# Kernel tuning notes

Measured on AMD Instinct MI355X. Metric: run time of the kernel, lower is better.

## Reference

```python
import jax, jax.numpy as jnp
import numpy as np

N = 100000   # nodes
E = 3200000  # edges
F = 128      # input features
H1 = 128     # first_gcn_dimensions
H2 = 64      # second_gcn_dimensions
D1 = 64      # first_dense_neurons
D2 = 8       # second_dense_neurons
L = 10       # number_of_labels


def setup_inputs() -> dict:
    key = jax.random.key(0)
    ks = jax.random.split(key, 8)
    edges = jax.random.randint(ks[0], (2, E), 0, N)
    features = jax.random.normal(ks[1], (N, F), dtype=jnp.float32)
    s = lambda k, shape: jax.random.normal(k, shape, dtype=jnp.float32) * 0.05
    return dict(
        edges=edges, features=features,
        W1=s(ks[2], (F, H1)), b1=jnp.zeros((H1,), jnp.float32),
        W2=s(ks[3], (H1, H2)), b2=jnp.zeros((H2,), jnp.float32),
        Wf1=s(ks[4], (H2, D1)), bf1=jnp.zeros((D1,), jnp.float32),
        Wf2=s(ks[5], (D1, D2)), bf2=jnp.zeros((D2,), jnp.float32),
        Wl=s(ks[6], (H2 * D2, L)), bl=jnp.zeros((L,), jnp.float32),
    )


def gcn_conv(x, W, b, src, dst, n):
    # PyG GCNConv: x' = D^{-1/2} (A + I) D^{-1/2} (x W) + b  (self-loops already in src/dst)
    h = x @ W                                            # [N, out]
    deg = jax.ops.segment_sum(jnp.ones(dst.shape[0], x.dtype), dst, num_segments=n)
    dinv = jnp.where(deg > 0, jax.lax.rsqrt(deg), 0.0)   # deg^{-1/2}, 0 for isolated
    norm = dinv[src] * dinv[dst]                         # [E+N]
    agg = jax.ops.segment_sum(h[src] * norm[:, None], dst, num_segments=n)
    return agg + b


def reference(edges, features, W1, b1, W2, b2, Wf1, bf1, Wf2, bf2, Wl, bl):
    n = features.shape[0]
    loop = jnp.arange(n)
    src = jnp.concatenate([edges[0], loop])
    dst = jnp.concatenate([edges[1], loop])

    h1 = jax.nn.relu(gcn_conv(features, W1, b1, src, dst, n))  # [N, H1]
    h2 = gcn_conv(h1, W2, b2, src, dst, n)                     # [N, H2]

    a1 = jnp.tanh(h2 @ Wf1 + bf1)                              # [N, D1]
    att = jax.nn.softmax(a1 @ Wf2 + bf2, axis=0)               # softmax over nodes, [N, D2]

    graph_embedding = (att.T @ h2).reshape(1, -1)              # [1, D2*H2]
    P = att.T @ att - jnp.eye(att.shape[1], dtype=att.dtype)   # [D2, D2]
    penalty = jnp.sum(jnp.sqrt(jnp.sum(P * P, axis=1)))

    predictions = jax.nn.log_softmax(graph_embedding @ Wl + bl, axis=1)  # [1, L]
    return graph_embedding, penalty, predictions
```

## Files before the change

kernel.cpp:

```cpp
#include <hip/hip_runtime.h>
#include <hip/hip_bf16.h>
#include <math.h>

#define NNODES 100000
#define NEDGES 3200000
#define NBUK ((NNODES + 127) >> 7)
#define NCHUNK 256
#define EPC (NEDGES / NCHUNK)
#define NPAD 100352
#define SLICEB ((size_t)NPAD * 32)

typedef float floatx2 __attribute__((ext_vector_type(2)));
typedef float f32x4 __attribute__((ext_vector_type(4)));
typedef short bf16x8 __attribute__((ext_vector_type(8)));

__device__ __forceinline__ unsigned short f2bf(float x) {
    unsigned u = __float_as_uint(x);
    unsigned r = u + 0x7FFFu + ((u >> 16) & 1u);
    return (unsigned short)(r >> 16);
}

__device__ __forceinline__ void acc8_fp8(uint2 v, floatx2* a) {
    a[0] += __builtin_amdgcn_cvt_pk_f32_fp8(v.x, false);
    a[1] += __builtin_amdgcn_cvt_pk_f32_fp8(v.x, true);
    a[2] += __builtin_amdgcn_cvt_pk_f32_fp8(v.y, false);
    a[3] += __builtin_amdgcn_cvt_pk_f32_fp8(v.y, true);
}

__global__ void prep_w_kernel(const float* __restrict__ W1, const float* __restrict__ W2,
                              unsigned short* __restrict__ Wt1, unsigned short* __restrict__ Wt2) {
    int i = blockIdx.x * 256 + threadIdx.x;
    if (i < 128 * 128) {
        int k = i >> 7, n = i & 127;
        Wt1[n * 128 + k] = f2bf(W1[i]);
    } else if (i < 128 * 128 + 128 * 64) {
        int j = i - 128 * 128;
        int k = j >> 6, n = j & 63;
        Wt2[n * 128 + k] = f2bf(W2[j]);
    }
}

__global__ __launch_bounds__(1024) void chunk_hist_kernel(const int* __restrict__ dst,
                                                          int* __restrict__ hist) {
    __shared__ int h[NBUK];
    int c = blockIdx.x, t = threadIdx.x;
    for (int i = t; i < NBUK; i += 1024) h[i] = 0;
    __syncthreads();
    const int4* d4 = (const int4*)(dst + c * EPC);
    for (int i = t; i < EPC / 4; i += 1024) {
        int4 d = d4[i];
        atomicAdd(&h[d.x >> 7], 1);
        atomicAdd(&h[d.y >> 7], 1);
        atomicAdd(&h[d.z >> 7], 1);
        atomicAdd(&h[d.w >> 7], 1);
    }
    __syncthreads();
    for (int i = t; i < NBUK; i += 1024)
        hist[c * NBUK + i] = h[i];
}

__global__ __launch_bounds__(256) void col_scan_kernel(int* __restrict__ hist,
                                                       int* __restrict__ btot) {
    __shared__ int sdat[NCHUNK];
    int b = blockIdx.x;
    int t = threadIdx.x;
    int v = hist[t * NBUK + b];
    sdat[t] = v;
    __syncthreads();
#pragma unroll
    for (int off = 1; off < NCHUNK; off <<= 1) {
        int x = (t >= off) ? sdat[t - off] : 0;
        __syncthreads();
        sdat[t] += x;
        __syncthreads();
    }
    hist[t * NBUK + b] = sdat[t] - v;
    if (t == NCHUNK - 1) btot[b] = sdat[t];
}

__global__ void bucket_scan_kernel(const int* __restrict__ btot, int* __restrict__ bstart,
                                   int* __restrict__ row_start, float* __restrict__ smalls) {
    __shared__ int s[1024];
    int t = threadIdx.x;
    if (t < 592) smalls[t] = 0.0f;
    int v = (t < NBUK) ? btot[t] : 0;
    s[t] = v;
    __syncthreads();
    for (int off = 1; off < 1024; off <<= 1) {
        int x = (t >= off) ? s[t - off] : 0;
        __syncthreads();
        s[t] += x;
        __syncthreads();
    }
    if (t < NBUK) bstart[t] = s[t] - v;
    if (t == 0) {
        bstart[NBUK] = NEDGES;
        row_start[NNODES] = NEDGES;
    }
}

__global__ __launch_bounds__(1024) void chunk_scatter_kernel(const int* __restrict__ src,
                                                             const int* __restrict__ dst,
                                                             const int* __restrict__ hist,
                                                             const int* __restrict__ bstart,
                                                             int* __restrict__ ebuk) {
    __shared__ int cur[NBUK];
    int c = blockIdx.x, t = threadIdx.x;
    for (int i = t; i < NBUK; i += 1024)
        cur[i] = bstart[i] + hist[c * NBUK + i];
    __syncthreads();
    const int4* s4 = (const int4*)(src + c * EPC);
    const int4* d4 = (const int4*)(dst + c * EPC);
    for (int i = t; i < EPC / 4; i += 1024) {
        int4 s = s4[i];
        int4 d = d4[i];
        int p0 = atomicAdd(&cur[d.x >> 7], 1);
        ebuk[p0] = s.x | ((d.x & 127) << 20);
        int p1 = atomicAdd(&cur[d.y >> 7], 1);
        ebuk[p1] = s.y | ((d.y & 127) << 20);
        int p2 = atomicAdd(&cur[d.z >> 7], 1);
        ebuk[p2] = s.z | ((d.z & 127) << 20);
        int p3 = atomicAdd(&cur[d.w >> 7], 1);
        ebuk[p3] = s.w | ((d.w & 127) << 20);
    }
}

__global__ __launch_bounds__(256) void build_kernel(const int* __restrict__ ebuk,
                                                    const int* __restrict__ bstart,
                                                    int* __restrict__ row_start,
                                                    float* __restrict__ dinv,
                                                    int* __restrict__ csr) {
    __shared__ int cnt[128];
    __shared__ int scn[128];
    __shared__ int cur[128];
    int b = blockIdx.x;
    int t = threadIdx.x;
    int s0 = bstart[b], s1 = bstart[b + 1];
    if (t < 128) cnt[t] = 0;
    __syncthreads();
    for (int i = s0 + t; i < s1; i += 256)
        atomicAdd(&cnt[(ebuk[i] >> 20) & 127], 1);
    __syncthreads();
    if (t < 128) scn[t] = cnt[t];
    __syncthreads();
#pragma unroll
    for (int off = 1; off < 128; off <<= 1) {
        int x = (t < 128 && t >= off) ? scn[t - off] : 0;
        __syncthreads();
        if (t < 128) scn[t] += x;
        __syncthreads();
    }
    int node = b * 128 + t;
    if (t < 128) {
        int rs = s0 + scn[t] - cnt[t];
        cur[t] = rs;
        if (node < NNODES) {
            row_start[node] = rs;
            dinv[node] = rsqrtf((float)cnt[t] + 1.0f);
        }
    }
    __syncthreads();
    for (int i = s0 + t; i < s1; i += 256) {
        int v = ebuk[i];
        int pos = atomicAdd(&cur[(v >> 20) & 127], 1);
        csr[pos] = v & 0xFFFFF;
    }
}

template <int KIN, int KOUT, bool ABF16>
__global__ __launch_bounds__(256) void gemm_mfma_kernel(const void* __restrict__ Av,
                                                        const unsigned short* __restrict__ Wt,
                                                        const float* __restrict__ rowscale,
                                                        unsigned char* __restrict__ stage) {
    constexpr int LDK = KIN + 8;
    constexpr int LDC = KOUT + 4;
    constexpr int SH_AB = (64 + KOUT) * LDK * 2;
    constexpr int SH_C  = 64 * LDC * 4;
    constexpr int SH = SH_AB > SH_C ? SH_AB : SH_C;
    __shared__ char shbuf[SH];
    unsigned short* As = (unsigned short*)shbuf;
    unsigned short* Ws = As + 64 * LDK;
    float* Cs = (float*)shbuf;
    int t = threadIdx.x;
    int block_row = blockIdx.x * 64;

    for (int idx = t; idx < KOUT * (KIN / 8); idx += 256) {
        int n = idx / (KIN / 8), c = idx % (KIN / 8);
        *(uint4*)(Ws + n * LDK + c * 8) = *(const uint4*)(Wt + n * KIN + c * 8);
    }
    if (ABF16) {
        const unsigned short* A = (const unsigned short*)Av;
        for (int idx = t; idx < 64 * (KIN / 8); idx += 256) {
            int r = idx / (KIN / 8), c = idx % (KIN / 8);
            uint4 v = make_uint4(0, 0, 0, 0);
            if (block_row + r < NNODES)
                v = *(const uint4*)(A + (size_t)(block_row + r) * KIN + c * 8);
            *(uint4*)(As + r * LDK + c * 8) = v;
        }
    } else {
        const float* A = (const float*)Av;
        for (int idx = t; idx < 64 * (KIN / 4); idx += 256) {
            int r = idx / (KIN / 4), c = idx % (KIN / 4);
            float4 v = make_float4(0.f, 0.f, 0.f, 0.f);
            if (block_row + r < NNODES)
                v = *(const float4*)(A + (size_t)(block_row + r) * KIN + c * 4);
            unsigned p0 = (unsigned)f2bf(v.x) | ((unsigned)f2bf(v.y) << 16);
            unsigned p1 = (unsigned)f2bf(v.z) | ((unsigned)f2bf(v.w) << 16);
            *(uint2*)(As + r * LDK + c * 4) = make_uint2(p0, p1);
        }
    }
    __syncthreads();

    int wv = t >> 6, lane = t & 63;
    int r0 = wv * 16;
    int m = lane & 15, q = lane >> 4;
    constexpr int NT = KOUT / 16;
    constexpr int KS = KIN / 32;
    f32x4 acc[NT];
#pragma unroll
    for (int nt = 0; nt < NT; nt++) acc[nt] = (f32x4)(0.f);
    bf16x8 afr[KS];
#pragma unroll
    for (int ks = 0; ks < KS; ks++)
        afr[ks] = *(bf16x8*)(As + (r0 + m) * LDK + ks * 32 + q * 8);
#pragma unroll
    for (int nt = 0; nt < NT; nt++) {
#pragma unroll
        for (int ks = 0; ks < KS; ks++) {
            bf16x8 b = *(bf16x8*)(Ws + (nt * 16 + m) * LDK + ks * 32 + q * 8);
            acc[nt] = __builtin_amdgcn_mfma_f32_16x16x32_bf16(afr[ks], b, acc[nt], 0, 0, 0);
        }
    }
    __syncthreads();
#pragma unroll
    for (int nt = 0; nt < NT; nt++)
#pragma unroll
        for (int j = 0; j < 4; j++)
            Cs[(r0 + q * 4 + j) * LDC + nt * 16 + m] = acc[nt][j];
    __syncthreads();
    for (int idx = t; idx < 64 * (KOUT / 4); idx += 256) {
        int r = idx / (KOUT / 4), c4 = idx % (KOUT / 4);
        int row = block_row + r;
        if (row < NNODES) {
            float4 v = *(float4*)(Cs + r * LDC + c4 * 4);
            float d = rowscale[row];
            int pk = __builtin_amdgcn_cvt_pk_fp8_f32(v.x * d, v.y * d, 0, false);
            pk = __builtin_amdgcn_cvt_pk_fp8_f32(v.z * d, v.w * d, pk, true);
            *(unsigned*)(stage + (size_t)(c4 >> 3) * SLICEB
                               + ((size_t)row << 5) + ((c4 & 7) << 2)) = (unsigned)pk;
        }
    }
}

template <int S, bool L1OUT>
__global__ __launch_bounds__(256) void gather_slice_kernel(
    const unsigned char* __restrict__ hs, const int* __restrict__ row_start,
    const int* __restrict__ csr, const float* __restrict__ dinv,
    const float* __restrict__ bias, void* __restrict__ outv) {
    int t = threadIdx.x;
    int wave = t >> 6, lane = t & 63;
    int s = (int)(blockIdx.x % S);
    int nb = (int)(blockIdx.x / S);
    int gn = lane >> 4, es = (lane >> 2) & 3, c = lane & 3;
    int node = nb * 16 + wave * 4 + gn;
    const unsigned char* hss = hs + (size_t)s * SLICEB;
    unsigned boff = (unsigned)c << 3;
    int start = row_start[node], end = row_start[node + 1];
    floatx2 acc[4];
#pragma unroll
    for (int i = 0; i < 4; i++) acc[i] = (floatx2)(0.f);
    int e = start + es;
    for (; e + 28 < end; e += 32) {
        int i0 = csr[e];      int i1 = csr[e + 4];
        int i2 = csr[e + 8];  int i3 = csr[e + 12];
        int i4 = csr[e + 16]; int i5 = csr[e + 20];
        int i6 = csr[e + 24]; int i7 = csr[e + 28];
        uint2 v0 = *(const uint2*)(hss + (((unsigned)i0 << 5) + boff));
        uint2 v1 = *(const uint2*)(hss + (((unsigned)i1 << 5) + boff));
        uint2 v2 = *(const uint2*)(hss + (((unsigned)i2 << 5) + boff));
        uint2 v3 = *(const uint2*)(hss + (((unsigned)i3 << 5) + boff));
        uint2 v4 = *(const uint2*)(hss + (((unsigned)i4 << 5) + boff));
        uint2 v5 = *(const uint2*)(hss + (((unsigned)i5 << 5) + boff));
        uint2 v6 = *(const uint2*)(hss + (((unsigned)i6 << 5) + boff));
        uint2 v7 = *(const uint2*)(hss + (((unsigned)i7 << 5) + boff));
        acc8_fp8(v0, acc); acc8_fp8(v1, acc); acc8_fp8(v2, acc); acc8_fp8(v3, acc);
        acc8_fp8(v4, acc); acc8_fp8(v5, acc); acc8_fp8(v6, acc); acc8_fp8(v7, acc);
    }
    for (; e + 4 < end; e += 8) {
        int i0 = csr[e];
        int i1 = csr[e + 4];
        uint2 v0 = *(const uint2*)(hss + (((unsigned)i0 << 5) + boff));
        uint2 v1 = *(const uint2*)(hss + (((unsigned)i1 << 5) + boff));
        acc8_fp8(v0, acc); acc8_fp8(v1, acc);
    }
    if (e < end) {
        uint2 v = *(const uint2*)(hss + (((unsigned)csr[e] << 5) + boff));
        acc8_fp8(v, acc);
    }
#pragma unroll
    for (int off = 4; off <= 8; off <<= 1)
#pragma unroll
        for (int i = 0; i < 4; i++) {
            acc[i].x += __shfl_xor(acc[i].x, off);
            acc[i].y += __shfl_xor(acc[i].y, off);
        }
    if (es == 0) {
        floatx2 sf[4];
#pragma unroll
        for (int i = 0; i < 4; i++) sf[i] = (floatx2)(0.f);
        acc8_fp8(*(const uint2*)(hss + (((unsigned)node << 5) + boff)), sf);
        float d = dinv[node];
        int j = s * 32 + c * 8;
        float4 b0 = *(const float4*)(bias + j);
        float4 b1 = *(const float4*)(bias + j + 4);
        float r0 = (acc[0].x + sf[0].x) * d + b0.x;
        float r1 = (acc[0].y + sf[0].y) * d + b0.y;
        float r2 = (acc[1].x + sf[1].x) * d + b0.z;
        float r3 = (acc[1].y + sf[1].y) * d + b0.w;
        float r4 = (acc[2].x + sf[2].x) * d + b1.x;
        float r5 = (acc[2].y + sf[2].y) * d + b1.y;
        float r6 = (acc[3].x + sf[3].x) * d + b1.z;
        float r7 = (acc[3].y + sf[3].y) * d + b1.w;
        if (L1OUT) {
            r0 = fmaxf(r0, 0.f); r1 = fmaxf(r1, 0.f);
            r2 = fmaxf(r2, 0.f); r3 = fmaxf(r3, 0.f);
            r4 = fmaxf(r4, 0.f); r5 = fmaxf(r5, 0.f);
            r6 = fmaxf(r6, 0.f); r7 = fmaxf(r7, 0.f);
            uint4 p;
            p.x = (unsigned)f2bf(r0) | ((unsigned)f2bf(r1) << 16);
            p.y = (unsigned)f2bf(r2) | ((unsigned)f2bf(r3) << 16);
            p.z = (unsigned)f2bf(r4) | ((unsigned)f2bf(r5) << 16);
            p.w = (unsigned)f2bf(r6) | ((unsigned)f2bf(r7) << 16);
            *(uint4*)((unsigned short*)outv + ((size_t)node << 7) + j) = p;
        } else {
            float* op = (float*)outv + ((size_t)node << 6) + j;
            *(float4*)op = make_float4(r0, r1, r2, r3);
            *(float4*)(op + 4) = make_float4(r4, r5, r6, r7);
        }
    }
}

__global__ __launch_bounds__(256) void attnpool_kernel(const float* __restrict__ h2,
                                                       const float* __restrict__ Wf1,
                                                       const float* __restrict__ bf1,
                                                       const float* __restrict__ Wf2,
                                                       const float* __restrict__ bf2,
                                                       float* __restrict__ ge,
                                                       float* __restrict__ ata,
                                                       float* __restrict__ colsum) {
    __shared__ float h2S[64][68];
    __shared__ float a1S[64][68];
    __shared__ float attS[64][8];
    __shared__ float colS[8][64];
    int t = threadIdx.x;
    int d0 = t >> 6;
    int j  = t & 63;
    int de = t >> 3, ee = t & 7;
    float accge0 = 0.f, accge1 = 0.f, accata = 0.f, acccol = 0.f;
    int ntiles = (NNODES + 63) / 64;
    for (int tile = blockIdx.x; tile < ntiles; tile += gridDim.x) {
        int base = tile * 64;
#pragma unroll
        for (int q = 0; q < 4; q++) {
            int idx = t + q * 256;
            int r = idx >> 4, cc = (idx & 15) * 4;
            int row = base + r;
            float4 v = (row < NNODES) ? *(const float4*)(h2 + (size_t)row * 64 + cc)
                                      : make_float4(0.f, 0.f, 0.f, 0.f);
            *(float4*)(&h2S[r][cc]) = v;
        }
        __syncthreads();
        {
            int cg = t & 15, rg = t >> 4;
            int jj = cg * 4, r0 = rg * 4;
            float4 b4 = *(const float4*)(bf1 + jj);
            float4 acc[4];
#pragma unroll
            for (int r = 0; r < 4; r++) acc[r] = b4;
#pragma unroll 4
            for (int k = 0; k < 64; k++) {
                float4 wv = *(const float4*)(Wf1 + (size_t)k * 64 + jj);
#pragma unroll
                for (int r = 0; r < 4; r++) {
                    float a = h2S[r0 + r][k];
                    acc[r].x += a * wv.x; acc[r].y += a * wv.y;
                    acc[r].z += a * wv.z; acc[r].w += a * wv.w;
                }
            }
#pragma unroll
            for (int r = 0; r < 4; r++) {
                a1S[r0 + r][jj]     = tanhf(acc[r].x);
                a1S[r0 + r][jj + 1] = tanhf(acc[r].y);
                a1S[r0 + r][jj + 2] = tanhf(acc[r].z);
                a1S[r0 + r][jj + 3] = tanhf(acc[r].w);
            }
        }
        __syncthreads();
        {
            int cc = t & 7, r = t >> 3;
#pragma unroll
            for (int h = 0; h < 2; h++) {
                int rr = r + h * 32;
                float acc = bf2[cc];
                for (int k = 0; k < 64; k++)
                    acc += a1S[rr][k] * Wf2[(size_t)k * 8 + cc];
                float ev = (base + rr < NNODES) ? __expf(acc) : 0.f;
                attS[rr][cc] = ev;
                colS[cc][rr] = ev;
            }
        }
        __syncthreads();
#pragma unroll 8
        for (int i = 0; i < 64; i++) {
            float hv = h2S[i][j];
            accge0 += attS[i][d0] * hv;
            accge1 += attS[i][d0 + 4] * hv;
        }
        if (t < 64) {
#pragma unroll 8
            for (int i = 0; i < 64; i++) accata += attS[i][de] * attS[i][ee];
        }
        if (t < 8) {
            float s = 0.f;
#pragma unroll
            for (int r = 0; r < 64; r++) s += colS[t][r];
            acccol += s;
        }
        __syncthreads();
    }
    atomicAdd(ge + d0 * 64 + j, accge0);
    atomicAdd(ge + (d0 + 4) * 64 + j, accge1);
    if (t < 64) atomicAdd(ata + de * 8 + ee, accata);
    if (t < 8) atomicAdd(colsum + t, acccol);
}

__global__ void final_kernel(const float* __restrict__ geacc, const float* __restrict__ ata,
                             const float* __restrict__ colsum, const float* __restrict__ Wl,
                             const float* __restrict__ bl, float* __restrict__ out) {
    __shared__ float geF[512];
    __shared__ float inv[8];
    __shared__ float logits[10];
    int t = threadIdx.x;
    if (t < 8) inv[t] = 1.0f / colsum[t];
    __syncthreads();
    for (int idx = t; idx < 512; idx += 64) {
        int d = idx >> 6;
        float v = geacc[idx] * inv[d];
        geF[idx] = v;
        out[idx] = v;
    }
    __syncthreads();
    if (t == 0) {
        float pen = 0.f;
        for (int d = 0; d < 8; d++) {
            float s = 0.f;
            for (int e = 0; e < 8; e++) {
                float p = ata[d * 8 + e] * inv[d] * inv[e] - (d == e ? 1.0f : 0.0f);
                s += p * p;
            }
            pen += sqrtf(s);
        }
        out[512] = pen;
    }
    if (t < 10) {
        float acc = bl[t];
        for (int k = 0; k < 512; k++) acc += geF[k] * Wl[(size_t)k * 10 + t];
        logits[t] = acc;
    }
    __syncthreads();
    if (t == 0) {
        float m = -INFINITY;
        for (int l = 0; l < 10; l++) m = fmaxf(m, logits[l]);
        float s = 0.f;
        for (int l = 0; l < 10; l++) s += expf(logits[l] - m);
        float ls = logf(s);
        for (int l = 0; l < 10; l++) out[513 + l] = logits[l] - m - ls;
    }
}

extern "C" void kernel_launch(void* const* d_in, const int* in_sizes, int n_in,
                              void* d_out, int out_size, void* d_ws, size_t ws_size,
                              hipStream_t stream) {
    const int* esrc = (const int*)d_in[0];
    const int* edst = esrc + NEDGES;
    const float* X   = (const float*)d_in[1];
    const float* W1  = (const float*)d_in[2];
    const float* b1  = (const float*)d_in[3];
    const float* W2  = (const float*)d_in[4];
    const float* b2  = (const float*)d_in[5];
    const float* Wf1 = (const float*)d_in[6];
    const float* bf1 = (const float*)d_in[7];
    const float* Wf2 = (const float*)d_in[8];
    const float* bf2 = (const float*)d_in[9];
    const float* Wl  = (const float*)d_in[10];
    const float* bl  = (const float*)d_in[11];
    float* out = (float*)d_out;

    float* ws     = (float*)d_ws;
    float* dinv   = ws;
    float* smalls = ws + 100352;
    float* colsum = smalls + 8;
    float* ata    = smalls + 16;
    float* geacc  = smalls + 80;
    float* A = ws + 101376;
    float* B = A + (size_t)NNODES * 128;
    int* row_start = (int*)(B + (size_t)NNODES * 128);
    int* btot      = row_start + 100352;
    int* bstart    = btot + 1024;
    int* csr       = bstart + 1024;
    unsigned short* Wt1 = (unsigned short*)(csr + NEDGES);
    unsigned short* Wt2 = Wt1 + 128 * 128;
    int* ebuk      = (int*)A;
    int* hist      = (int*)B;
    unsigned char* stage = (unsigned char*)A;
    unsigned short* h1 = (unsigned short*)B;
    float* h2  = B;

    prep_w_kernel<<<96, 256, 0, stream>>>(W1, W2, Wt1, Wt2);

    chunk_hist_kernel<<<NCHUNK, 1024, 0, stream>>>(edst, hist);
    col_scan_kernel<<<NBUK, 256, 0, stream>>>(hist, btot);
    bucket_scan_kernel<<<1, 1024, 0, stream>>>(btot, bstart, row_start, smalls);
    chunk_scatter_kernel<<<NCHUNK, 1024, 0, stream>>>(esrc, edst, hist, bstart, ebuk);
    build_kernel<<<NBUK, 256, 0, stream>>>(ebuk, bstart, row_start, dinv, csr);

    gemm_mfma_kernel<128, 128, false><<<(NNODES + 63) / 64, 256, 0, stream>>>(X, Wt1, dinv, stage);
    gather_slice_kernel<4, true><<<(NNODES / 16) * 4, 256, 0, stream>>>(stage, row_start, csr, dinv, b1, h1);

    gemm_mfma_kernel<128, 64, true><<<(NNODES + 63) / 64, 256, 0, stream>>>(h1, Wt2, dinv, stage);
    gather_slice_kernel<2, false><<<(NNODES / 16) * 2, 256, 0, stream>>>(stage, row_start, csr, dinv, b2, h2);

    attnpool_kernel<<<512, 256, 0, stream>>>(h2, Wf1, bf1, Wf2, bf2, geacc, ata, colsum);
    final_kernel<<<1, 64, 0, stream>>>(geacc, ata, colsum, Wl, bl, out);
}
```

Measured before the change: 426.0 us.

## Use row-major fp8 staging and one-wave-per-node gather for first GCN layer

For the 128-wide first layer, the GEMM epilogue now writes fp8 rows contiguously (128 bytes per node) instead of four 32-byte column slices. A new gather kernel assigns one wave per node: 16 lanes cover the full row and 4 lane groups split the edges. Loads are unrolled 16-deep, followed by a cross-group shuffle reduction and a fused self-loop, bias, ReLU and bf16 store. The aim is for each neighbor fetch to be a full 128-byte line and for the CSR list to be read once rather than once per slice, at the cost of a less L2-friendly working set per pass.

```diff
diff --git a/kernel.cpp b/kernel.cpp
--- a/kernel.cpp
+++ b/kernel.cpp
@@ -246,9 +246,109 @@
             float d = rowscale[row];
             int pk = __builtin_amdgcn_cvt_pk_fp8_f32(v.x * d, v.y * d, 0, false);
             pk = __builtin_amdgcn_cvt_pk_fp8_f32(v.z * d, v.w * d, pk, true);
-            *(unsigned*)(stage + (size_t)(c4 >> 3) * SLICEB
-                               + ((size_t)row << 5) + ((c4 & 7) << 2)) = (unsigned)pk;
-        }
+            if constexpr (KOUT == 64) {
+                *(unsigned*)(stage + (size_t)(c4 >> 3) * SLICEB
+                                   + ((size_t)row << 5) + ((c4 & 7) << 2)) = (unsigned)pk;
+            } else {
+                *(unsigned*)(stage + (size_t)row * KOUT + c4 * 4) = (unsigned)pk;
+            }
+        }
+    }
+}
+
+__global__ __launch_bounds__(256) void gather128_kernel(
+    const unsigned char* __restrict__ hs, const int* __restrict__ row_start,
+    const int* __restrict__ csr, const float* __restrict__ dinv,
+    const float* __restrict__ bias, unsigned short* __restrict__ out) {
+    int wave = threadIdx.x >> 6;
+    int lane = threadIdx.x & 63;
+    int n = blockIdx.x * 4 + wave;
+    if (n >= NNODES) return;
+    int g = lane >> 4;
+    int c = lane & 15;
+    unsigned boff = (unsigned)c << 3;
+    int start = row_start[n], end = row_start[n + 1];
+    floatx2 acc[4];
+#pragma unroll
+    for (int i = 0; i < 4; i++) acc[i] = (floatx2)(0.f);
+    int w = (start + 3) & ~3;
+    if (w > end) w = end;
+    {
+        int e2 = start + g;
+        if (e2 < w) {
+            unsigned o = ((unsigned)csr[e2] << 7) + boff;
+            acc8_fp8(*(const uint2*)(hs + o), acc);
+        }
+    }
+    for (; w + 64 <= end; w += 64) {
+        const int* cp = csr + w + 16 * g;
+        int4 ca = *(const int4*)(cp);
+        int4 cb = *(const int4*)(cp + 4);
+        int4 cc = *(const int4*)(cp + 8);
+        int4 cd = *(const int4*)(cp + 12);
+        uint2 v0  = *(const uint2*)(hs + (((unsigned)ca.x << 7) + boff));
+        uint2 v1  = *(const uint2*)(hs + (((unsigned)ca.y << 7) + boff));
+        uint2 v2  = *(const uint2*)(hs + (((unsigned)ca.z << 7) + boff));
+        uint2 v3  = *(const uint2*)(hs + (((unsigned)ca.w << 7) + boff));
+        uint2 v4  = *(const uint2*)(hs + (((unsigned)cb.x << 7) + boff));
+        uint2 v5  = *(const uint2*)(hs + (((unsigned)cb.y << 7) + boff));
+        uint2 v6  = *(const uint2*)(hs + (((unsigned)cb.z << 7) + boff));
+        uint2 v7  = *(const uint2*)(hs + (((unsigned)cb.w << 7) + boff));
+        uint2 v8  = *(const uint2*)(hs + (((unsigned)cc.x << 7) + boff));
+        uint2 v9  = *(const uint2*)(hs + (((unsigned)cc.y << 7) + boff));
+        uint2 v10 = *(const uint2*)(hs + (((unsigned)cc.z << 7) + boff));
+        uint2 v11 = *(const uint2*)(hs + (((unsigned)cc.w << 7) + boff));
+        uint2 v12 = *(const uint2*)(hs + (((unsigned)cd.x << 7) + boff));
+        uint2 v13 = *(const uint2*)(hs + (((unsigned)cd.y << 7) + boff));
+        uint2 v14 = *(const uint2*)(hs + (((unsigned)cd.z << 7) + boff));
+        uint2 v15 = *(const uint2*)(hs + (((unsigned)cd.w << 7) + boff));
+        acc8_fp8(v0, acc);  acc8_fp8(v1, acc);  acc8_fp8(v2, acc);  acc8_fp8(v3, acc);
+        acc8_fp8(v4, acc);  acc8_fp8(v5, acc);  acc8_fp8(v6, acc);  acc8_fp8(v7, acc);
+        acc8_fp8(v8, acc);  acc8_fp8(v9, acc);  acc8_fp8(v10, acc); acc8_fp8(v11, acc);
+        acc8_fp8(v12, acc); acc8_fp8(v13, acc); acc8_fp8(v14, acc); acc8_fp8(v15, acc);
+    }
+    for (; w + 16 <= end; w += 16) {
+        int4 cs = *(const int4*)(csr + w + 4 * g);
+        uint2 v0 = *(const uint2*)(hs + (((unsigned)cs.x << 7) + boff));
+        uint2 v1 = *(const uint2*)(hs + (((unsigned)cs.y << 7) + boff));
+        uint2 v2 = *(const uint2*)(hs + (((unsigned)cs.z << 7) + boff));
+        uint2 v3 = *(const uint2*)(hs + (((unsigned)cs.w << 7) + boff));
+        acc8_fp8(v0, acc); acc8_fp8(v1, acc); acc8_fp8(v2, acc); acc8_fp8(v3, acc);
+    }
+    for (int e2 = w + g; e2 < end; e2 += 4) {
+        unsigned o = ((unsigned)csr[e2] << 7) + boff;
+        acc8_fp8(*(const uint2*)(hs + o), acc);
+    }
+#pragma unroll
+    for (int off = 16; off <= 32; off <<= 1)
+#pragma unroll
+        for (int i = 0; i < 4; i++) {
+            acc[i].x += __shfl_xor(acc[i].x, off);
+            acc[i].y += __shfl_xor(acc[i].y, off);
+        }
+    if (g == 0) {
+        floatx2 s[4];
+#pragma unroll
+        for (int i = 0; i < 4; i++) s[i] = (floatx2)(0.f);
+        acc8_fp8(*(const uint2*)(hs + (((unsigned)n << 7) + boff)), s);
+        float d = dinv[n];
+        int j = c * 8;
+        float4 b0 = *(const float4*)(bias + j);
+        float4 b1 = *(const float4*)(bias + j + 4);
+        float r0 = fmaxf((acc[0].x + s[0].x) * d + b0.x, 0.f);
+        float r1 = fmaxf((acc[0].y + s[0].y) * d + b0.y, 0.f);
+        float r2 = fmaxf((acc[1].x + s[1].x) * d + b0.z, 0.f);
+        float r3 = fmaxf((acc[1].y + s[1].y) * d + b0.w, 0.f);
+        float r4 = fmaxf((acc[2].x + s[2].x) * d + b1.x, 0.f);
+        float r5 = fmaxf((acc[2].y + s[2].y) * d + b1.y, 0.f);
+        float r6 = fmaxf((acc[3].x + s[3].x) * d + b1.z, 0.f);
+        float r7 = fmaxf((acc[3].y + s[3].y) * d + b1.w, 0.f);
+        uint4 p;
+        p.x = (unsigned)f2bf(r0) | ((unsigned)f2bf(r1) << 16);
+        p.y = (unsigned)f2bf(r2) | ((unsigned)f2bf(r3) << 16);
+        p.z = (unsigned)f2bf(r4) | ((unsigned)f2bf(r5) << 16);
+        p.w = (unsigned)f2bf(r6) | ((unsigned)f2bf(r7) << 16);
+        *(uint4*)(out + (((size_t)n << 7) + j)) = p;
     }
 }
 
@@ -525,7 +625,7 @@
     build_kernel<<<NBUK, 256, 0, stream>>>(ebuk, bstart, row_start, dinv, csr);
 
     gemm_mfma_kernel<128, 128, false><<<(NNODES + 63) / 64, 256, 0, stream>>>(X, Wt1, dinv, stage);
-    gather_slice_kernel<4, true><<<(NNODES / 16) * 4, 256, 0, stream>>>(stage, row_start, csr, dinv, b1, h1);
+    gather128_kernel<<<(NNODES + 3) / 4, 256, 0, stream>>>(stage, row_start, csr, dinv, b1, h1);
 
     gemm_mfma_kernel<128, 64, true><<<(NNODES + 63) / 64, 256, 0, stream>>>(h1, Wt2, dinv, stage);
     gather_slice_kernel<2, false><<<(NNODES / 16) * 2, 256, 0, stream>>>(stage, row_start, csr, dinv, b2, h2);
```

New measurement: 401.3 us. 1.06x faster.
